# Performance work log

Measured on AMD Instinct MI355X. Metric: run time of the kernel, lower is better.

## Reference

```python
import jax, jax.numpy as jnp
import numpy as np

N_NODES = 100000
N_EDGES = 1600000
N_GRAPHS = 64
IN_CH, HID_CH, OUT_CH, N_CLS = 128, 128, 64, 2


def setup_inputs() -> dict:
    key = jax.random.key(0)
    ks = jax.random.split(key, 8)
    x = jax.random.normal(ks[0], (N_NODES, IN_CH), dtype=jnp.float32)
    edge_index = jax.random.randint(ks[1], (2, N_EDGES), 0, N_NODES)
    batch = jnp.sort(jax.random.randint(ks[2], (N_NODES,), 0, N_GRAPHS))
    glorot = lambda k, shp: jax.random.normal(k, shp, dtype=jnp.float32) / np.float32(np.sqrt(shp[0]))
    return {
        "x": x, "edge_index": edge_index, "batch": batch,
        "W1": glorot(ks[3], (IN_CH, HID_CH)), "b1": jnp.zeros((HID_CH,), jnp.float32),
        "W2": glorot(ks[4], (HID_CH, HID_CH)), "b2": jnp.zeros((HID_CH,), jnp.float32),
        "W3": glorot(ks[5], (HID_CH, OUT_CH)), "b3": jnp.zeros((OUT_CH,), jnp.float32),
        "Wfc": glorot(ks[6], (OUT_CH, N_CLS)), "bfc": jnp.zeros((N_CLS,), jnp.float32),
    }


def gcn_conv(x, src, dst, W, b):
    """PyG GCNConv: add self-loops, D^{-1/2} (A+I) D^{-1/2} (x W) + b."""
    n = x.shape[0]
    h = x @ W  # [N, out]
    # degree with self-loops: 1 + in-degree at dst
    deg = jnp.ones((n,), h.dtype).at[dst].add(1.0)
    dinv = jax.lax.rsqrt(deg)  # deg >= 1 always (self-loop)
    norm = dinv[src] * dinv[dst]  # [E]
    agg = jnp.zeros_like(h).at[dst].add(h[src] * norm[:, None])
    agg = agg + h * (dinv * dinv)[:, None]  # self-loop messages
    return agg + b


def global_mean_pool(x, batch, num_graphs):
    s = jax.ops.segment_sum(x, batch, num_segments=num_graphs)
    cnt = jax.ops.segment_sum(jnp.ones((x.shape[0],), x.dtype), batch, num_segments=num_graphs)
    return s / jnp.maximum(cnt, 1.0)[:, None]


def reference(x, edge_index, batch, W1, b1, W2, b2, W3, b3, Wfc, bfc):
    src, dst = edge_index[0], edge_index[1]
    h = jax.nn.relu(gcn_conv(x, src, dst, W1, b1))   # dropout p=0.0 (eval) -> identity
    h = jax.nn.relu(gcn_conv(h, src, dst, W2, b2))
    h = gcn_conv(h, src, dst, W3, b3)
    g = global_mean_pool(h, batch, N_GRAPHS)          # [G, OUT_CH]
    return g @ Wfc + bfc                              # [G, N_CLS]
```

## Files before the change

kernel.cpp:

```cpp
#include <hip/hip_runtime.h>
#include <hip/hip_bf16.h>


#define THREADS 256
#define BSHIFT 9
#define BSIZE 512

typedef __attribute__((ext_vector_type(8))) short short8;
typedef __attribute__((ext_vector_type(16))) float floatx16;

__device__ __forceinline__ unsigned f2bf(float f) {
    unsigned u = __float_as_uint(f);
    return (u + 0x7fffu + ((u >> 16) & 1u)) >> 16;
}

__device__ __forceinline__ void bf8_acc(uint4 v, float* ac) {
    ac[0] += __uint_as_float(v.x << 16);
    ac[1] += __uint_as_float(v.x & 0xffff0000u);
    ac[2] += __uint_as_float(v.y << 16);
    ac[3] += __uint_as_float(v.y & 0xffff0000u);
    ac[4] += __uint_as_float(v.z << 16);
    ac[5] += __uint_as_float(v.z & 0xffff0000u);
    ac[6] += __uint_as_float(v.w << 16);
    ac[7] += __uint_as_float(v.w & 0xffff0000u);
}


__global__ __launch_bounds__(THREADS) void bucket_count(const int* __restrict__ dst,
                                                        int* __restrict__ btotal,
                                                        int E, int nbuck) {
    __shared__ int cnt[BSIZE];
    for (int i = threadIdx.x; i < nbuck; i += THREADS) cnt[i] = 0;
    __syncthreads();
    for (int e = blockIdx.x * THREADS + threadIdx.x; e < E; e += gridDim.x * THREADS)
        atomicAdd(&cnt[dst[e] >> BSHIFT], 1);
    __syncthreads();
    for (int i = threadIdx.x; i < nbuck; i += THREADS) {
        int c = cnt[i];
        if (c) atomicAdd(&btotal[i], c);
    }
}

__global__ __launch_bounds__(512) void bucket_scan(const int* __restrict__ btotal,
                                                   int* __restrict__ bbase,
                                                   int* __restrict__ bcursor,
                                                   float* __restrict__ gsum,
                                                   float* __restrict__ zrow,
                                                   int nbuck, int E) {
    __shared__ int lds[512];
    int t = threadIdx.x;
    for (int i = t; i < 64 * 64; i += 512) gsum[i] = 0.0f;
    if (t < 64) zrow[t] = 0.0f;
    int v = (t < nbuck) ? btotal[t] : 0;
    lds[t] = v;
    __syncthreads();
    for (int off = 1; off < 512; off <<= 1) {
        int tv = (t >= off) ? lds[t - off] : 0;
        __syncthreads();
        lds[t] += tv;
        __syncthreads();
    }
    if (t < nbuck) {
        int excl = lds[t] - v;
        bbase[t] = excl;
        bcursor[t] = excl;
    }
    if (t == 0) bbase[nbuck] = E;
}

__global__ __launch_bounds__(THREADS) void bucket_scatter(const int* __restrict__ src,
                                                          const int* __restrict__ dst,
                                                          int* __restrict__ bcursor,
                                                          int* __restrict__ pairs, int E) {
    __shared__ int cnt[BSIZE];
    __shared__ int base[BSIZE];
    for (int i = threadIdx.x; i < BSIZE; i += THREADS) cnt[i] = 0;
    __syncthreads();
    int e0 = blockIdx.x * 2048;
    int myb[8], myrank[8], mypk[8];
#pragma unroll
    for (int j = 0; j < 8; ++j) {
        int e = e0 + j * THREADS + threadIdx.x;
        myb[j] = -1;
        if (e < E) {
            int d = dst[e];
            mypk[j] = (src[e] << BSHIFT) | (d & (BSIZE - 1));
            myb[j] = d >> BSHIFT;
            myrank[j] = atomicAdd(&cnt[myb[j]], 1);
        }
    }
    __syncthreads();
    for (int i = threadIdx.x; i < BSIZE; i += THREADS) {
        int c = cnt[i];
        base[i] = c ? atomicAdd(&bcursor[i], c) : 0;
    }
    __syncthreads();
#pragma unroll
    for (int j = 0; j < 8; ++j)
        if (myb[j] >= 0) pairs[(size_t)base[myb[j]] + myrank[j]] = mypk[j];
}

__global__ __launch_bounds__(512) void bucket_fill(const int* __restrict__ pairs,
                                                   const int* __restrict__ bbase,
                                                   int* __restrict__ row_start,
                                                   float* __restrict__ dinv,
                                                   int* __restrict__ esrc,
                                                   int N, int E, int nbuck) {
    __shared__ int cnt[BSIZE];
    __shared__ int scn[BSIZE];
    int b = blockIdx.x, t = threadIdx.x;
    int s = bbase[b], e = bbase[b + 1];
    cnt[t] = 0;
    __syncthreads();
    for (int i = s + t; i < e; i += 512) atomicAdd(&cnt[pairs[i] & (BSIZE - 1)], 1);
    __syncthreads();
    int v = cnt[t];
    scn[t] = v;
    __syncthreads();
    for (int off = 1; off < 512; off <<= 1) {
        int tv = (t >= off) ? scn[t - off] : 0;
        __syncthreads();
        scn[t] += tv;
        __syncthreads();
    }
    int excl = scn[t] - v;
    int g = (b << BSHIFT) + t;
    if (g < N) {
        row_start[g] = s + excl;
        dinv[g] = rsqrtf(1.0f + (float)v);
    }
    if (b == nbuck - 1 && t == 0) row_start[N] = E;
    scn[t] = excl;
    __syncthreads();
    for (int i = s + t; i < e; i += 512) {
        int p = pairs[i];
        int r = atomicAdd(&scn[p & (BSIZE - 1)], 1);
        esrc[s + r] = ((unsigned)p) >> BSHIFT;
    }
}

__device__ __forceinline__ void wt_pack(const float* W, uint4* Wtp, int C, int li) {
    int c = li >> 4, ch = li & 15;
    unsigned r[8];
#pragma unroll
    for (int j = 0; j < 8; ++j) r[j] = f2bf(W[(size_t)(ch * 8 + j) * C + c]);
    uint4 o;
    o.x = r[0] | (r[1] << 16);
    o.y = r[2] | (r[3] << 16);
    o.z = r[4] | (r[5] << 16);
    o.w = r[6] | (r[7] << 16);
    Wtp[li] = o;
}

__global__ __launch_bounds__(THREADS) void prep_wt_all(const float* __restrict__ W1,
                                                       const float* __restrict__ W2,
                                                       const float* __restrict__ W3,
                                                       uint4* __restrict__ Wt1,
                                                       uint4* __restrict__ Wt2,
                                                       uint4* __restrict__ Wt3) {
    int idx = blockIdx.x * THREADS + threadIdx.x;
    if (idx < 2048) wt_pack(W1, Wt1, 128, idx);
    else if (idx < 4096) wt_pack(W2, Wt2, 128, idx - 2048);
    else if (idx < 5120) wt_pack(W3, Wt3, 64, idx - 4096);
}

__global__ __launch_bounds__(THREADS) void prep_x(const float* __restrict__ x,
                                                  const float* __restrict__ dinv,
                                                  uint4* __restrict__ Z, int n) {
    int idx = blockIdx.x * THREADS + threadIdx.x;
    if (idx >= n * 16) return;
    int r = idx >> 4, c = idx & 15;
    float dv = dinv[r];
    const float* p = x + (size_t)r * 128 + c * 8;
    float4 a = *(const float4*)p;
    float4 b = *(const float4*)(p + 4);
    uint4 o;
    o.x = f2bf(a.x * dv) | (f2bf(a.y * dv) << 16);
    o.y = f2bf(a.z * dv) | (f2bf(a.w * dv) << 16);
    o.z = f2bf(b.x * dv) | (f2bf(b.y * dv) << 16);
    o.w = f2bf(b.z * dv) | (f2bf(b.w * dv) << 16);
    Z[idx] = o;
}

__global__ __launch_bounds__(THREADS) void fused_layer(const uint4* __restrict__ Z,
                                                       const uint4* __restrict__ Wt,
                                                       const int* __restrict__ row_start,
                                                       const int* __restrict__ esrc,
                                                       const float* __restrict__ dinv,
                                                       const float* __restrict__ bias,
                                                       const uint4* __restrict__ zrow,
                                                       uint4* __restrict__ out, int n) {
    __shared__ __align__(16) uint4 ldsX[64 * 16];
    int row0 = blockIdx.x * 64;
    int maxr = n - row0;
    if (maxr > 64) maxr = 64;
    int tid = threadIdx.x;
    int lane = tid & 15, grp = tid >> 4;
    const uint4* zl = zrow + lane;

    for (int round = 0; round < 4; ++round) {
        int r = round * 16 + grp;
        int node = row0 + r;
        int nd = (node < n) ? node : (n - 1);
        float ac[8] = {0, 0, 0, 0, 0, 0, 0, 0};
        bf8_acc(Z[(size_t)nd * 16 + lane], ac);
        float dv = dinv[nd];
        int s = row_start[nd], e = row_start[nd + 1];
        int i = s;
        int nmain = (e - s) >> 3;
        if (nmain > 0) {
            int s0 = esrc[i], s1 = esrc[i + 1], s2 = esrc[i + 2], s3 = esrc[i + 3];
            int s4 = esrc[i + 4], s5 = esrc[i + 5], s6 = esrc[i + 6], s7 = esrc[i + 7];
            for (int m = 0; m < nmain; ++m) {
                uint4 v0 = Z[(size_t)s0 * 16 + lane];
                uint4 v1 = Z[(size_t)s1 * 16 + lane];
                uint4 v2 = Z[(size_t)s2 * 16 + lane];
                uint4 v3 = Z[(size_t)s3 * 16 + lane];
                uint4 v4 = Z[(size_t)s4 * 16 + lane];
                uint4 v5 = Z[(size_t)s5 * 16 + lane];
                uint4 v6 = Z[(size_t)s6 * 16 + lane];
                uint4 v7 = Z[(size_t)s7 * 16 + lane];
                int ni = i + 8;
                int t0 = esrc[ni], t1 = esrc[ni + 1], t2 = esrc[ni + 2], t3 = esrc[ni + 3];
                int t4 = esrc[ni + 4], t5 = esrc[ni + 5], t6 = esrc[ni + 6], t7 = esrc[ni + 7];
                bf8_acc(v0, ac); bf8_acc(v1, ac); bf8_acc(v2, ac); bf8_acc(v3, ac);
                bf8_acc(v4, ac); bf8_acc(v5, ac); bf8_acc(v6, ac); bf8_acc(v7, ac);
                s0 = t0; s1 = t1; s2 = t2; s3 = t3;
                s4 = t4; s5 = t5; s6 = t6; s7 = t7;
                i = ni;
            }
        }
        if (i < e) {
            const uint4* p0 = (i + 0 < e) ? (Z + ((size_t)esrc[i + 0] * 16 + lane)) : zl;
            const uint4* p1 = (i + 1 < e) ? (Z + ((size_t)esrc[i + 1] * 16 + lane)) : zl;
            const uint4* p2 = (i + 2 < e) ? (Z + ((size_t)esrc[i + 2] * 16 + lane)) : zl;
            const uint4* p3 = (i + 3 < e) ? (Z + ((size_t)esrc[i + 3] * 16 + lane)) : zl;
            const uint4* p4 = (i + 4 < e) ? (Z + ((size_t)esrc[i + 4] * 16 + lane)) : zl;
            const uint4* p5 = (i + 5 < e) ? (Z + ((size_t)esrc[i + 5] * 16 + lane)) : zl;
            const uint4* p6 = (i + 6 < e) ? (Z + ((size_t)esrc[i + 6] * 16 + lane)) : zl;
            const uint4* p7 = (i + 7 < e) ? (Z + ((size_t)esrc[i + 7] * 16 + lane)) : zl;
            uint4 v0 = *p0; uint4 v1 = *p1; uint4 v2 = *p2; uint4 v3 = *p3;
            uint4 v4 = *p4; uint4 v5 = *p5; uint4 v6 = *p6; uint4 v7 = *p7;
            bf8_acc(v0, ac); bf8_acc(v1, ac); bf8_acc(v2, ac); bf8_acc(v3, ac);
            bf8_acc(v4, ac); bf8_acc(v5, ac); bf8_acc(v6, ac); bf8_acc(v7, ac);
        }
        uint4 o;
        o.x = f2bf(ac[0] * dv) | (f2bf(ac[1] * dv) << 16);
        o.y = f2bf(ac[2] * dv) | (f2bf(ac[3] * dv) << 16);
        o.z = f2bf(ac[4] * dv) | (f2bf(ac[5] * dv) << 16);
        o.w = f2bf(ac[6] * dv) | (f2bf(ac[7] * dv) << 16);
        ldsX[r * 16 + (lane ^ (r & 7))] = o;
    }
    __syncthreads();

    int l = tid & 63, wv = tid >> 6;
    int l31 = l & 31, half = l >> 5;
    int nt = wv & 1, mt0 = (wv >> 1) * 2;
    floatx16 acc[2];
#pragma unroll
    for (int t = 0; t < 2; ++t)
#pragma unroll
        for (int q = 0; q < 16; ++q) acc[t][q] = 0.0f;
    int xrow = nt * 32 + l31, xsw = xrow & 7;
#pragma unroll
    for (int kt = 0; kt < 8; ++kt) {
        int chunk = kt * 2 + half;
        short8 xf = *(const short8*)&ldsX[xrow * 16 + (chunk ^ xsw)];
#pragma unroll
        for (int t = 0; t < 2; ++t) {
            int c = (mt0 + t) * 32 + l31;
            short8 wf = *(const short8*)&Wt[c * 16 + chunk];
            acc[t] = __builtin_amdgcn_mfma_f32_32x32x16_bf16(wf, xf, acc[t], 0, 0, 0);
        }
    }
    __syncthreads();

    int node = nt * 32 + l31;
    float dv = (node < maxr) ? dinv[row0 + node] : 0.0f;
    char* outb = (char*)ldsX;
#pragma unroll
    for (int t = 0; t < 2; ++t) {
        int cb = (mt0 + t) * 32;
#pragma unroll
        for (int q = 0; q < 4; ++q) {
            float v[4];
#pragma unroll
            for (int m = 0; m < 4; ++m) {
                int ch = cb + 8 * q + 4 * half + m;
                float x_ = acc[t][q * 4 + m] + bias[ch];
                x_ = fmaxf(x_, 0.0f);
                v[m] = x_ * dv;
            }
            uint2 pk = make_uint2(f2bf(v[0]) | (f2bf(v[1]) << 16),
                                  f2bf(v[2]) | (f2bf(v[3]) << 16));
            int chunk = (cb >> 3) + q;
            *(uint2*)(outb + node * 256 + ((chunk ^ (node & 7)) * 16) + half * 8) = pk;
        }
    }
    __syncthreads();
    for (int idx = tid; idx < maxr * 16; idx += THREADS) {
        int r = idx >> 4, c = idx & 15;
        out[(size_t)(row0 + r) * 16 + c] = *(uint4*)(outb + r * 256 + ((c ^ (r & 7)) * 16));
    }
}

__global__ __launch_bounds__(THREADS) void gemm3(const uint4* __restrict__ Z,
                                                 const uint4* __restrict__ Wt,
                                                 uint4* __restrict__ out, int n) {
    __shared__ __align__(16) uint4 ldsX[64 * 16];
    int row0 = blockIdx.x * 64;
    int maxr = n - row0;
    if (maxr > 64) maxr = 64;
    int tid = threadIdx.x;
    for (int idx = tid; idx < 1024; idx += THREADS) {
        int r = idx >> 4, c = idx & 15;
        uint4 o = (r < maxr) ? Z[(size_t)(row0 + r) * 16 + c] : make_uint4(0, 0, 0, 0);
        ldsX[r * 16 + (c ^ (r & 7))] = o;
    }
    __syncthreads();
    int l = tid & 63, wv = tid >> 6;
    int l31 = l & 31, half = l >> 5;
    int nt = wv & 1, mt = wv >> 1;
    floatx16 acc;
#pragma unroll
    for (int q = 0; q < 16; ++q) acc[q] = 0.0f;
    int xrow = nt * 32 + l31, xsw = xrow & 7;
#pragma unroll
    for (int kt = 0; kt < 8; ++kt) {
        int chunk = kt * 2 + half;
        short8 xf = *(const short8*)&ldsX[xrow * 16 + (chunk ^ xsw)];
        int c = mt * 32 + l31;
        short8 wf = *(const short8*)&Wt[c * 16 + chunk];
        acc = __builtin_amdgcn_mfma_f32_32x32x16_bf16(wf, xf, acc, 0, 0, 0);
    }
    __syncthreads();
    int node = nt * 32 + l31;
    char* outb = (char*)ldsX;
    int cb = mt * 32;
#pragma unroll
    for (int q = 0; q < 4; ++q) {
        uint2 pk = make_uint2(f2bf(acc[q * 4 + 0]) | (f2bf(acc[q * 4 + 1]) << 16),
                              f2bf(acc[q * 4 + 2]) | (f2bf(acc[q * 4 + 3]) << 16));
        int chunk = (cb >> 3) + q;
        *(uint2*)(outb + node * 128 + ((chunk ^ (node & 7)) * 16) + half * 8) = pk;
    }
    __syncthreads();
    for (int idx = tid; idx < maxr * 8; idx += THREADS) {
        int r = idx >> 3, c = idx & 7;
        out[(size_t)(row0 + r) * 8 + c] = *(uint4*)(outb + r * 128 + ((c ^ (r & 7)) * 16));
    }
}

__global__ __launch_bounds__(THREADS) void agg_pool(const uint4* __restrict__ Ps,
                                                    const int* __restrict__ row_start,
                                                    const int* __restrict__ esrc,
                                                    const float* __restrict__ dinv,
                                                    const float* __restrict__ bias,
                                                    const int* __restrict__ batch,
                                                    const uint4* __restrict__ zrow,
                                                    float* __restrict__ gsum, int n) {
    __shared__ float gpart[32][65];
    __shared__ int used[32];
    int tid = threadIdx.x;
    int lane = tid & 7, grp = tid >> 3;
    int node = blockIdx.x * 32 + grp;
    if (tid < 32) used[tid] = 0;
    for (int idx = tid; idx < 2048; idx += THREADS) gpart[idx >> 6][idx & 63] = 0.0f;
    __syncthreads();
    int gmin = batch[blockIdx.x * 32];
    const uint4* zl = zrow + lane;
    if (node < n) {
        float ac[8] = {0, 0, 0, 0, 0, 0, 0, 0};
        bf8_acc(Ps[(size_t)node * 8 + lane], ac);
        float dv = dinv[node];
        int s = row_start[node], e = row_start[node + 1];
        int i = s;
        int nmain = (e - s) >> 3;
        if (nmain > 0) {
            int s0 = esrc[i], s1 = esrc[i + 1], s2 = esrc[i + 2], s3 = esrc[i + 3];
            int s4 = esrc[i + 4], s5 = esrc[i + 5], s6 = esrc[i + 6], s7 = esrc[i + 7];
            for (int m = 0; m < nmain; ++m) {
                uint4 v0 = Ps[(size_t)s0 * 8 + lane];
                uint4 v1 = Ps[(size_t)s1 * 8 + lane];
                uint4 v2 = Ps[(size_t)s2 * 8 + lane];
                uint4 v3 = Ps[(size_t)s3 * 8 + lane];
                uint4 v4 = Ps[(size_t)s4 * 8 + lane];
                uint4 v5 = Ps[(size_t)s5 * 8 + lane];
                uint4 v6 = Ps[(size_t)s6 * 8 + lane];
                uint4 v7 = Ps[(size_t)s7 * 8 + lane];
                int ni = i + 8;
                int t0 = esrc[ni], t1 = esrc[ni + 1], t2 = esrc[ni + 2], t3 = esrc[ni + 3];
                int t4 = esrc[ni + 4], t5 = esrc[ni + 5], t6 = esrc[ni + 6], t7 = esrc[ni + 7];
                bf8_acc(v0, ac); bf8_acc(v1, ac); bf8_acc(v2, ac); bf8_acc(v3, ac);
                bf8_acc(v4, ac); bf8_acc(v5, ac); bf8_acc(v6, ac); bf8_acc(v7, ac);
                s0 = t0; s1 = t1; s2 = t2; s3 = t3;
                s4 = t4; s5 = t5; s6 = t6; s7 = t7;
                i = ni;
            }
        }
        if (i < e) {
            const uint4* p0 = (i + 0 < e) ? (Ps + ((size_t)esrc[i + 0] * 8 + lane)) : zl;
            const uint4* p1 = (i + 1 < e) ? (Ps + ((size_t)esrc[i + 1] * 8 + lane)) : zl;
            const uint4* p2 = (i + 2 < e) ? (Ps + ((size_t)esrc[i + 2] * 8 + lane)) : zl;
            const uint4* p3 = (i + 3 < e) ? (Ps + ((size_t)esrc[i + 3] * 8 + lane)) : zl;
            const uint4* p4 = (i + 4 < e) ? (Ps + ((size_t)esrc[i + 4] * 8 + lane)) : zl;
            const uint4* p5 = (i + 5 < e) ? (Ps + ((size_t)esrc[i + 5] * 8 + lane)) : zl;
            const uint4* p6 = (i + 6 < e) ? (Ps + ((size_t)esrc[i + 6] * 8 + lane)) : zl;
            const uint4* p7 = (i + 7 < e) ? (Ps + ((size_t)esrc[i + 7] * 8 + lane)) : zl;
            uint4 v0 = *p0; uint4 v1 = *p1; uint4 v2 = *p2; uint4 v3 = *p3;
            uint4 v4 = *p4; uint4 v5 = *p5; uint4 v6 = *p6; uint4 v7 = *p7;
            bf8_acc(v0, ac); bf8_acc(v1, ac); bf8_acc(v2, ac); bf8_acc(v3, ac);
            bf8_acc(v4, ac); bf8_acc(v5, ac); bf8_acc(v6, ac); bf8_acc(v7, ac);
        }
        float4 b0 = ((const float4*)bias)[lane * 2];
        float4 b1 = ((const float4*)bias)[lane * 2 + 1];
        float h[8];
        h[0] = fmaf(dv, ac[0], b0.x); h[1] = fmaf(dv, ac[1], b0.y);
        h[2] = fmaf(dv, ac[2], b0.z); h[3] = fmaf(dv, ac[3], b0.w);
        h[4] = fmaf(dv, ac[4], b1.x); h[5] = fmaf(dv, ac[5], b1.y);
        h[6] = fmaf(dv, ac[6], b1.z); h[7] = fmaf(dv, ac[7], b1.w);
        int g = batch[node];
        int slot = g - gmin;
        if (slot < 32) {
            if (lane == 0) used[slot] = 1;
#pragma unroll
            for (int j = 0; j < 8; ++j) atomicAdd(&gpart[slot][lane * 8 + j], h[j]);
        } else {
#pragma unroll
            for (int j = 0; j < 8; ++j) atomicAdd(&gsum[(size_t)g * 64 + lane * 8 + j], h[j]);
        }
    }
    __syncthreads();
    for (int idx = tid; idx < 2048; idx += THREADS) {
        int s = idx >> 6, ch = idx & 63;
        if (used[s]) atomicAdd(&gsum[(size_t)(gmin + s) * 64 + ch], gpart[s][ch]);
    }
}

__device__ __forceinline__ int dev_lower_bound(const int* a, int n, int key) {
    int lo = 0, hi = n;
    while (lo < hi) {
        int mid = (lo + hi) >> 1;
        if (a[mid] < key) lo = mid + 1;
        else hi = mid;
    }
    return lo;
}

__global__ __launch_bounds__(128) void finalize_fc(const float* __restrict__ gsum,
                                                   const int* __restrict__ batch, int n,
                                                   const float* __restrict__ Wfc,
                                                   const float* __restrict__ bfc,
                                                   float* __restrict__ out) {
    __shared__ float gm[64 * 64];
    __shared__ float cnt[64];
    int t = threadIdx.x;
    if (t < 64)
        cnt[t] = (float)(dev_lower_bound(batch, n, t + 1) - dev_lower_bound(batch, n, t));
    __syncthreads();
    for (int i = t; i < 64 * 64; i += 128) gm[i] = gsum[i] / fmaxf(cnt[i >> 6], 1.0f);
    __syncthreads();
    int g = t >> 1, cls = t & 1;
    float acc = bfc[cls];
    for (int c = 0; c < 64; ++c) acc = fmaf(gm[g * 64 + c], Wfc[c * 2 + cls], acc);
    out[g * 2 + cls] = acc;
}

extern "C" void kernel_launch(void* const* d_in, const int* in_sizes, int n_in,
                              void* d_out, int out_size, void* d_ws, size_t ws_size,
                              hipStream_t stream) {
    const float* x    = (const float*)d_in[0];
    const int*   ei   = (const int*)d_in[1];
    const int*   batch= (const int*)d_in[2];
    const float* W1   = (const float*)d_in[3];
    const float* b1   = (const float*)d_in[4];
    const float* W2   = (const float*)d_in[5];
    const float* b2   = (const float*)d_in[6];
    const float* W3   = (const float*)d_in[7];
    const float* b3   = (const float*)d_in[8];
    const float* Wfc  = (const float*)d_in[9];
    const float* bfc  = (const float*)d_in[10];
    float* out = (float*)d_out;

    const int N = in_sizes[2];
    const int E = in_sizes[1] / 2;
    const int* esrc_in = ei;
    const int* edst_in = ei + E;
    const int nbuck = (N + BSIZE - 1) >> BSHIFT;

    uint4* bufA      = (uint4*)d_ws;
    uint4* bufB      = bufA + (size_t)N * 16;
    uint4* bufC      = bufB + (size_t)N * 16;
    int*   pairs     = (int*)(bufC + (size_t)N * 8);
    int*   esrc      = pairs + E;
    int*   row_start = esrc + E;
    float* dinv      = (float*)(row_start + N + 1);
    int*   btotal    = (int*)(dinv + N);
    int*   bbase     = btotal + 512;
    int*   bcursor   = bbase + 513;
    float* gsum      = (float*)(bcursor + 512);
    uint4* Wt1       = (uint4*)(gsum + 64 * 64);
    uint4* Wt2       = Wt1 + 2048;
    uint4* Wt3       = Wt2 + 2048;
    float* zrow      = (float*)(Wt3 + 1024);

    hipMemsetAsync(btotal, 0, 512 * sizeof(int), stream);
    bucket_count<<<512, THREADS, 0, stream>>>(edst_in, btotal, E, nbuck);
    bucket_scan<<<1, 512, 0, stream>>>(btotal, bbase, bcursor, gsum, zrow, nbuck, E);
    bucket_scatter<<<(E + 2047) / 2048, THREADS, 0, stream>>>(esrc_in, edst_in, bcursor, pairs, E);
    bucket_fill<<<nbuck, 512, 0, stream>>>(pairs, bbase, row_start, dinv, esrc, N, E, nbuck);
    prep_wt_all<<<20, THREADS, 0, stream>>>(W1, W2, W3, Wt1, Wt2, Wt3);
    prep_x<<<(N * 16 + THREADS - 1) / THREADS, THREADS, 0, stream>>>(x, dinv, bufA, N);

    const int GB = (N + 63) / 64;

    fused_layer<<<GB, THREADS, 0, stream>>>(bufA, Wt1, row_start, esrc, dinv, b1,
                                            (const uint4*)zrow, bufB, N);
    fused_layer<<<GB, THREADS, 0, stream>>>(bufB, Wt2, row_start, esrc, dinv, b2,
                                            (const uint4*)zrow, bufA, N);
    gemm3<<<GB, THREADS, 0, stream>>>(bufA, Wt3, bufC, N);
    agg_pool<<<(N + 31) / 32, THREADS, 0, stream>>>(bufC, row_start, esrc, dinv, b3, batch,
                                                    (const uint4*)zrow, gsum, N);

    finalize_fc<<<1, 128, 0, stream>>>(gsum, batch, N, Wfc, bfc, out);
}
```

Measured before the change: 422.2 us.

## Fuse layer-3 GEMM into second fused layer and add nontemporal loads/stores

Removes the separate gemm3 kernel by computing the layer-3 projection inside the second fused_layer, reusing the layer-2 output already held in LDS. This saves one kernel launch plus a full read of the layer-2 activations. Edge index streams (dst, src, esrc) now use nontemporal loads and the layer outputs use nontemporal stores, so streamed data should stop evicting the gathered feature rows from cache. The cost is extra MFMA work and two more LDS barriers in the second layer, and the nontemporal stores may hurt the next kernel if it could have read those outputs from L2.

```diff
diff --git a/kernel.cpp b/kernel.cpp
--- a/kernel.cpp
+++ b/kernel.cpp
@@ -8,6 +8,9 @@
 
 typedef __attribute__((ext_vector_type(8))) short short8;
 typedef __attribute__((ext_vector_type(16))) float floatx16;
+typedef __attribute__((ext_vector_type(4))) unsigned int uint32x4;
+
+#define NTL(p) __builtin_nontemporal_load(p)
 
 __device__ __forceinline__ unsigned f2bf(float f) {
     unsigned u = __float_as_uint(f);
@@ -33,7 +36,7 @@
     for (int i = threadIdx.x; i < nbuck; i += THREADS) cnt[i] = 0;
     __syncthreads();
     for (int e = blockIdx.x * THREADS + threadIdx.x; e < E; e += gridDim.x * THREADS)
-        atomicAdd(&cnt[dst[e] >> BSHIFT], 1);
+        atomicAdd(&cnt[NTL(dst + e) >> BSHIFT], 1);
     __syncthreads();
     for (int i = threadIdx.x; i < nbuck; i += THREADS) {
         int c = cnt[i];
@@ -83,8 +86,8 @@
         int e = e0 + j * THREADS + threadIdx.x;
         myb[j] = -1;
         if (e < E) {
-            int d = dst[e];
-            mypk[j] = (src[e] << BSHIFT) | (d & (BSIZE - 1));
+            int d = NTL(dst + e);
+            mypk[j] = (NTL(src + e) << BSHIFT) | (d & (BSIZE - 1));
             myb[j] = d >> BSHIFT;
             myrank[j] = atomicAdd(&cnt[myb[j]], 1);
         }
@@ -189,7 +192,9 @@
                                                        const float* __restrict__ dinv,
                                                        const float* __restrict__ bias,
                                                        const uint4* __restrict__ zrow,
-                                                       uint4* __restrict__ out, int n) {
+                                                       uint4* __restrict__ out,
+                                                       const uint4* __restrict__ WtP,
+                                                       uint4* __restrict__ outP, int n) {
     __shared__ __align__(16) uint4 ldsX[64 * 16];
     int row0 = blockIdx.x * 64;
     int maxr = n - row0;
@@ -209,8 +214,8 @@
         int i = s;
         int nmain = (e - s) >> 3;
         if (nmain > 0) {
-            int s0 = esrc[i], s1 = esrc[i + 1], s2 = esrc[i + 2], s3 = esrc[i + 3];
-            int s4 = esrc[i + 4], s5 = esrc[i + 5], s6 = esrc[i + 6], s7 = esrc[i + 7];
+            int s0 = NTL(esrc + i), s1 = NTL(esrc + i + 1), s2 = NTL(esrc + i + 2), s3 = NTL(esrc + i + 3);
+            int s4 = NTL(esrc + i + 4), s5 = NTL(esrc + i + 5), s6 = NTL(esrc + i + 6), s7 = NTL(esrc + i + 7);
             for (int m = 0; m < nmain; ++m) {
                 uint4 v0 = Z[(size_t)s0 * 16 + lane];
                 uint4 v1 = Z[(size_t)s1 * 16 + lane];
@@ -221,8 +226,8 @@
                 uint4 v6 = Z[(size_t)s6 * 16 + lane];
                 uint4 v7 = Z[(size_t)s7 * 16 + lane];
                 int ni = i + 8;
-                int t0 = esrc[ni], t1 = esrc[ni + 1], t2 = esrc[ni + 2], t3 = esrc[ni + 3];
-                int t4 = esrc[ni + 4], t5 = esrc[ni + 5], t6 = esrc[ni + 6], t7 = esrc[ni + 7];
+                int t0 = NTL(esrc + ni), t1 = NTL(esrc + ni + 1), t2 = NTL(esrc + ni + 2), t3 = NTL(esrc + ni + 3);
+                int t4 = NTL(esrc + ni + 4), t5 = NTL(esrc + ni + 5), t6 = NTL(esrc + ni + 6), t7 = NTL(esrc + ni + 7);
                 bf8_acc(v0, ac); bf8_acc(v1, ac); bf8_acc(v2, ac); bf8_acc(v3, ac);
                 bf8_acc(v4, ac); bf8_acc(v5, ac); bf8_acc(v6, ac); bf8_acc(v7, ac);
                 s0 = t0; s1 = t1; s2 = t2; s3 = t3;
@@ -231,14 +236,14 @@
             }
         }
         if (i < e) {
-            const uint4* p0 = (i + 0 < e) ? (Z + ((size_t)esrc[i + 0] * 16 + lane)) : zl;
-            const uint4* p1 = (i + 1 < e) ? (Z + ((size_t)esrc[i + 1] * 16 + lane)) : zl;
-            const uint4* p2 = (i + 2 < e) ? (Z + ((size_t)esrc[i + 2] * 16 + lane)) : zl;
-            const uint4* p3 = (i + 3 < e) ? (Z + ((size_t)esrc[i + 3] * 16 + lane)) : zl;
-            const uint4* p4 = (i + 4 < e) ? (Z + ((size_t)esrc[i + 4] * 16 + lane)) : zl;
-            const uint4* p5 = (i + 5 < e) ? (Z + ((size_t)esrc[i + 5] * 16 + lane)) : zl;
-            const uint4* p6 = (i + 6 < e) ? (Z + ((size_t)esrc[i + 6] * 16 + lane)) : zl;
-            const uint4* p7 = (i + 7 < e) ? (Z + ((size_t)esrc[i + 7] * 16 + lane)) : zl;
+            const uint4* p0 = (i + 0 < e) ? (Z + ((size_t)NTL(esrc + i + 0) * 16 + lane)) : zl;
+            const uint4* p1 = (i + 1 < e) ? (Z + ((size_t)NTL(esrc + i + 1) * 16 + lane)) : zl;
+            const uint4* p2 = (i + 2 < e) ? (Z + ((size_t)NTL(esrc + i + 2) * 16 + lane)) : zl;
+            const uint4* p3 = (i + 3 < e) ? (Z + ((size_t)NTL(esrc + i + 3) * 16 + lane)) : zl;
+            const uint4* p4 = (i + 4 < e) ? (Z + ((size_t)NTL(esrc + i + 4) * 16 + lane)) : zl;
+            const uint4* p5 = (i + 5 < e) ? (Z + ((size_t)NTL(esrc + i + 5) * 16 + lane)) : zl;
+            const uint4* p6 = (i + 6 < e) ? (Z + ((size_t)NTL(esrc + i + 6) * 16 + lane)) : zl;
+            const uint4* p7 = (i + 7 < e) ? (Z + ((size_t)NTL(esrc + i + 7) * 16 + lane)) : zl;
             uint4 v0 = *p0; uint4 v1 = *p1; uint4 v2 = *p2; uint4 v3 = *p3;
             uint4 v4 = *p4; uint4 v5 = *p5; uint4 v6 = *p6; uint4 v7 = *p7;
             bf8_acc(v0, ac); bf8_acc(v1, ac); bf8_acc(v2, ac); bf8_acc(v3, ac);
@@ -300,54 +305,38 @@
     __syncthreads();
     for (int idx = tid; idx < maxr * 16; idx += THREADS) {
         int r = idx >> 4, c = idx & 15;
-        out[(size_t)(row0 + r) * 16 + c] = *(uint4*)(outb + r * 256 + ((c ^ (r & 7)) * 16));
-    }
-}
-
-__global__ __launch_bounds__(THREADS) void gemm3(const uint4* __restrict__ Z,
-                                                 const uint4* __restrict__ Wt,
-                                                 uint4* __restrict__ out, int n) {
-    __shared__ __align__(16) uint4 ldsX[64 * 16];
-    int row0 = blockIdx.x * 64;
-    int maxr = n - row0;
-    if (maxr > 64) maxr = 64;
-    int tid = threadIdx.x;
-    for (int idx = tid; idx < 1024; idx += THREADS) {
-        int r = idx >> 4, c = idx & 15;
-        uint4 o = (r < maxr) ? Z[(size_t)(row0 + r) * 16 + c] : make_uint4(0, 0, 0, 0);
-        ldsX[r * 16 + (c ^ (r & 7))] = o;
-    }
-    __syncthreads();
-    int l = tid & 63, wv = tid >> 6;
-    int l31 = l & 31, half = l >> 5;
-    int nt = wv & 1, mt = wv >> 1;
-    floatx16 acc;
-#pragma unroll
-    for (int q = 0; q < 16; ++q) acc[q] = 0.0f;
-    int xrow = nt * 32 + l31, xsw = xrow & 7;
-#pragma unroll
-    for (int kt = 0; kt < 8; ++kt) {
-        int chunk = kt * 2 + half;
-        short8 xf = *(const short8*)&ldsX[xrow * 16 + (chunk ^ xsw)];
-        int c = mt * 32 + l31;
-        short8 wf = *(const short8*)&Wt[c * 16 + chunk];
-        acc = __builtin_amdgcn_mfma_f32_32x32x16_bf16(wf, xf, acc, 0, 0, 0);
-    }
-    __syncthreads();
-    int node = nt * 32 + l31;
-    char* outb = (char*)ldsX;
-    int cb = mt * 32;
-#pragma unroll
-    for (int q = 0; q < 4; ++q) {
-        uint2 pk = make_uint2(f2bf(acc[q * 4 + 0]) | (f2bf(acc[q * 4 + 1]) << 16),
-                              f2bf(acc[q * 4 + 2]) | (f2bf(acc[q * 4 + 3]) << 16));
-        int chunk = (cb >> 3) + q;
-        *(uint2*)(outb + node * 128 + ((chunk ^ (node & 7)) * 16) + half * 8) = pk;
-    }
-    __syncthreads();
-    for (int idx = tid; idx < maxr * 8; idx += THREADS) {
-        int r = idx >> 3, c = idx & 7;
-        out[(size_t)(row0 + r) * 8 + c] = *(uint4*)(outb + r * 128 + ((c ^ (r & 7)) * 16));
+        uint32x4 v = *(const uint32x4*)(outb + r * 256 + ((c ^ (r & 7)) * 16));
+        __builtin_nontemporal_store(v, (uint32x4*)(out + (size_t)(row0 + r) * 16 + c));
+    }
+
+    if (outP) {
+        floatx16 accp;
+#pragma unroll
+        for (int q = 0; q < 16; ++q) accp[q] = 0.0f;
+        int mt = wv >> 1;
+#pragma unroll
+        for (int kt = 0; kt < 8; ++kt) {
+            int chunk = kt * 2 + half;
+            short8 xf = *(const short8*)&ldsX[xrow * 16 + (chunk ^ xsw)];
+            int c = mt * 32 + l31;
+            short8 wf = *(const short8*)&WtP[c * 16 + chunk];
+            accp = __builtin_amdgcn_mfma_f32_32x32x16_bf16(wf, xf, accp, 0, 0, 0);
+        }
+        __syncthreads();
+        int cb = mt * 32;
+#pragma unroll
+        for (int q = 0; q < 4; ++q) {
+            uint2 pk = make_uint2(f2bf(accp[q * 4 + 0]) | (f2bf(accp[q * 4 + 1]) << 16),
+                                  f2bf(accp[q * 4 + 2]) | (f2bf(accp[q * 4 + 3]) << 16));
+            int chunk = (cb >> 3) + q;
+            *(uint2*)(outb + node * 128 + ((chunk ^ (node & 7)) * 16) + half * 8) = pk;
+        }
+        __syncthreads();
+        for (int idx = tid; idx < maxr * 8; idx += THREADS) {
+            int r = idx >> 3, c = idx & 7;
+            uint32x4 v = *(const uint32x4*)(outb + r * 128 + ((c ^ (r & 7)) * 16));
+            __builtin_nontemporal_store(v, (uint32x4*)(outP + (size_t)(row0 + r) * 8 + c));
+        }
     }
 }
 
@@ -377,8 +366,8 @@
         int i = s;
         int nmain = (e - s) >> 3;
         if (nmain > 0) {
-            int s0 = esrc[i], s1 = esrc[i + 1], s2 = esrc[i + 2], s3 = esrc[i + 3];
-            int s4 = esrc[i + 4], s5 = esrc[i + 5], s6 = esrc[i + 6], s7 = esrc[i + 7];
+            int s0 = NTL(esrc + i), s1 = NTL(esrc + i + 1), s2 = NTL(esrc + i + 2), s3 = NTL(esrc + i + 3);
+            int s4 = NTL(esrc + i + 4), s5 = NTL(esrc + i + 5), s6 = NTL(esrc + i + 6), s7 = NTL(esrc + i + 7);
             for (int m = 0; m < nmain; ++m) {
                 uint4 v0 = Ps[(size_t)s0 * 8 + lane];
                 uint4 v1 = Ps[(size_t)s1 * 8 + lane];
@@ -389,8 +378,8 @@
                 uint4 v6 = Ps[(size_t)s6 * 8 + lane];
                 uint4 v7 = Ps[(size_t)s7 * 8 + lane];
                 int ni = i + 8;
-                int t0 = esrc[ni], t1 = esrc[ni + 1], t2 = esrc[ni + 2], t3 = esrc[ni + 3];
-                int t4 = esrc[ni + 4], t5 = esrc[ni + 5], t6 = esrc[ni + 6], t7 = esrc[ni + 7];
+                int t0 = NTL(esrc + ni), t1 = NTL(esrc + ni + 1), t2 = NTL(esrc + ni + 2), t3 = NTL(esrc + ni + 3);
+                int t4 = NTL(esrc + ni + 4), t5 = NTL(esrc + ni + 5), t6 = NTL(esrc + ni + 6), t7 = NTL(esrc + ni + 7);
                 bf8_acc(v0, ac); bf8_acc(v1, ac); bf8_acc(v2, ac); bf8_acc(v3, ac);
                 bf8_acc(v4, ac); bf8_acc(v5, ac); bf8_acc(v6, ac); bf8_acc(v7, ac);
                 s0 = t0; s1 = t1; s2 = t2; s3 = t3;
@@ -399,14 +388,14 @@
             }
         }
         if (i < e) {
-            const uint4* p0 = (i + 0 < e) ? (Ps + ((size_t)esrc[i + 0] * 8 + lane)) : zl;
-            const uint4* p1 = (i + 1 < e) ? (Ps + ((size_t)esrc[i + 1] * 8 + lane)) : zl;
-            const uint4* p2 = (i + 2 < e) ? (Ps + ((size_t)esrc[i + 2] * 8 + lane)) : zl;
-            const uint4* p3 = (i + 3 < e) ? (Ps + ((size_t)esrc[i + 3] * 8 + lane)) : zl;
-            const uint4* p4 = (i + 4 < e) ? (Ps + ((size_t)esrc[i + 4] * 8 + lane)) : zl;
-            const uint4* p5 = (i + 5 < e) ? (Ps + ((size_t)esrc[i + 5] * 8 + lane)) : zl;
-            const uint4* p6 = (i + 6 < e) ? (Ps + ((size_t)esrc[i + 6] * 8 + lane)) : zl;
-            const uint4* p7 = (i + 7 < e) ? (Ps + ((size_t)esrc[i + 7] * 8 + lane)) : zl;
+            const uint4* p0 = (i + 0 < e) ? (Ps + ((size_t)NTL(esrc + i + 0) * 8 + lane)) : zl;
+            const uint4* p1 = (i + 1 < e) ? (Ps + ((size_t)NTL(esrc + i + 1) * 8 + lane)) : zl;
+            const uint4* p2 = (i + 2 < e) ? (Ps + ((size_t)NTL(esrc + i + 2) * 8 + lane)) : zl;
+            const uint4* p3 = (i + 3 < e) ? (Ps + ((size_t)NTL(esrc + i + 3) * 8 + lane)) : zl;
+            const uint4* p4 = (i + 4 < e) ? (Ps + ((size_t)NTL(esrc + i + 4) * 8 + lane)) : zl;
+            const uint4* p5 = (i + 5 < e) ? (Ps + ((size_t)NTL(esrc + i + 5) * 8 + lane)) : zl;
+            const uint4* p6 = (i + 6 < e) ? (Ps + ((size_t)NTL(esrc + i + 6) * 8 + lane)) : zl;
+            const uint4* p7 = (i + 7 < e) ? (Ps + ((size_t)NTL(esrc + i + 7) * 8 + lane)) : zl;
             uint4 v0 = *p0; uint4 v1 = *p1; uint4 v2 = *p2; uint4 v3 = *p3;
             uint4 v4 = *p4; uint4 v5 = *p5; uint4 v6 = *p6; uint4 v7 = *p7;
             bf8_acc(v0, ac); bf8_acc(v1, ac); bf8_acc(v2, ac); bf8_acc(v3, ac);
@@ -515,10 +504,9 @@
     const int GB = (N + 63) / 64;
 
     fused_layer<<<GB, THREADS, 0, stream>>>(bufA, Wt1, row_start, esrc, dinv, b1,
-                                            (const uint4*)zrow, bufB, N);
+                                            (const uint4*)zrow, bufB, nullptr, nullptr, N);
     fused_layer<<<GB, THREADS, 0, stream>>>(bufB, Wt2, row_start, esrc, dinv, b2,
-                                            (const uint4*)zrow, bufA, N);
-    gemm3<<<GB, THREADS, 0, stream>>>(bufA, Wt3, bufC, N);
+                                            (const uint4*)zrow, bufA, Wt3, bufC, N);
     agg_pool<<<(N + 31) / 32, THREADS, 0, stream>>>(bufC, row_start, esrc, dinv, b3, batch,
                                                     (const uint4*)zrow, gsum, N);
 
```

Measured after the change: 438.3 us. 3.8% more time.
